# Performance work log

Hardware: AMD Instinct MI355X
Metric: run time of the kernel (lower is better)

The kernel has to match this reference:

```python
import jax, jax.numpy as jnp
import numpy as np

MAX_THRESHOLD = 0.25  # init kwarg
B, S, D, E = 8, 4096, 512, 8


def setup_inputs() -> dict:
    key = jax.random.key(0)
    ks = jax.random.split(key, 5)
    scale = 1.0 / np.sqrt(D)
    return {
        "inputs": jax.random.normal(ks[0], (B, S, D), dtype=jnp.float32),
        "W_gate": jax.random.normal(ks[1], (D, E), dtype=jnp.float32) * scale,
        "b_gate": jnp.zeros((E,), dtype=jnp.float32),
        "W_thr": jax.random.normal(ks[2], (D, 1), dtype=jnp.float32) * scale,
        "b_thr": jnp.zeros((1,), dtype=jnp.float32),
        "W_exp": jax.random.normal(ks[3], (E, D, D), dtype=jnp.float32) * scale,
        "b_exp": jnp.zeros((E, D), dtype=jnp.float32),
    }


def reference(inputs, W_gate, b_gate, W_thr, b_thr, W_exp, b_exp):
    d = inputs.shape[-1]
    x = inputs.reshape(-1, d)  # [T, D]
    # gating
    gate_logits = jax.nn.softmax(x @ W_gate + b_gate, axis=-1)          # [T, E]
    thresholds = jax.nn.sigmoid(x @ W_thr + b_thr) * MAX_THRESHOLD      # [T, 1]
    adapted = gate_logits - thresholds                                  # [T, E]
    selected = (adapted >= 0).astype(x.dtype)                           # [T, E]
    weights = adapted * selected                                        # [T, E]
    wsum = jnp.sum(weights, axis=-1, keepdims=True)
    wsum = jnp.where(wsum == 0, jnp.ones_like(wsum), wsum)
    weights = weights / wsum
    # dense-equivalent of gather->expert->scatter (weights are 0 where unselected)
    ex_out = jnp.einsum('td,edf->etf', x, W_exp) + b_exp[:, None, :]    # [E, T, D]
    results = jnp.einsum('etf,te->tf', ex_out, weights)                 # [T, D]
    return results.reshape(inputs.shape[:-1] + (results.shape[-1],))
```

## Files before the change

### kernel.cpp

```cpp
#include <hip/hip_runtime.h>


#define T_TOKENS 32768
#define DDIM 512
#define KDIM 4096
#define SLOT32 8192

typedef __attribute__((ext_vector_type(8))) short short8;
typedef __attribute__((ext_vector_type(4))) float floatx4;
typedef __bf16 bf16x2 __attribute__((ext_vector_type(2)));

__device__ __forceinline__ unsigned short f2bf(float f) {
    unsigned int u = __float_as_uint(f);
    u += 0x7FFFu + ((u >> 16) & 1u);
    return (unsigned short)(u >> 16);
}

__device__ __forceinline__ unsigned int pk2(float a, float b) {
#if __has_builtin(__builtin_amdgcn_cvt_pk_bf16_f32)
    bf16x2 v = __builtin_amdgcn_cvt_pk_bf16_f32(a, b);
    return __builtin_bit_cast(unsigned int, v);
#else
    return (unsigned int)f2bf(a) | ((unsigned int)f2bf(b) << 16);
#endif
}

__device__ __forceinline__ void async_copy16(const void* g, void* l) {
    __builtin_amdgcn_global_load_lds(
        (const __attribute__((address_space(1))) void*)g,
        (__attribute__((address_space(3))) void*)l, 16, 0, 0);
}

__device__ __forceinline__ unsigned int scale_pair(unsigned int u, float w) {
    float lo = __uint_as_float(u << 16) * w;
    float hi = __uint_as_float(u & 0xFFFF0000u) * w;
    return pk2(lo, hi);
}

__global__ __launch_bounds__(256) void gating_cvt_bt(
    const float* __restrict__ x, const float* __restrict__ Wg,
    const float* __restrict__ bg, const float* __restrict__ Wt,
    const float* __restrict__ bt, float* __restrict__ wbuf,
    unsigned short* __restrict__ Xbf,
    const float* __restrict__ Wexp, unsigned short* __restrict__ Bt)
{
    const int tid = threadIdx.x;

    if (blockIdx.x >= 512) {
        __shared__ float tile[64][65];
        const int bb = blockIdx.x - 512;
        const int k0 = (bb & 63) * 64;
        const int n0 = (bb >> 6) * 64;
        const int r = tid >> 4, cq = tid & 15;
#pragma unroll
        for (int p = 0; p < 4; ++p) {
            const int rr = p * 16 + r;
            const float4 v = *(const float4*)(Wexp + (size_t)(k0 + rr) * 512 + n0 + cq * 4);
            tile[rr][cq * 4 + 0] = v.x;
            tile[rr][cq * 4 + 1] = v.y;
            tile[rr][cq * 4 + 2] = v.z;
            tile[rr][cq * 4 + 3] = v.w;
        }
        __syncthreads();
        const int rn = tid >> 2;
        const int kq = tid & 3;
        alignas(16) unsigned short buf[16];
#pragma unroll
        for (int j = 0; j < 16; ++j) buf[j] = f2bf(tile[kq * 16 + j][rn]);
        unsigned short* dst = Bt + (size_t)(n0 + rn) * KDIM + k0 + kq * 16;
        *(uint4*)(dst) = *(const uint4*)(buf);
        *(uint4*)(dst + 8) = *(const uint4*)(buf + 8);
        return;
    }

    const int wv = tid >> 6;
    const int lane = tid & 63;

    float4 wg[16];
    {
        const float4* wgp = (const float4*)(Wg + lane * 64);
#pragma unroll
        for (int c = 0; c < 16; ++c) wg[c] = wgp[c];
    }
    const float4 wt0 = *(const float4*)(Wt + lane * 8);
    const float4 wt1 = *(const float4*)(Wt + lane * 8 + 4);
    const float bgv[8] = {bg[0], bg[1], bg[2], bg[3], bg[4], bg[5], bg[6], bg[7]};
    const float btv = bt[0];

    for (int it = 0; it < 16; ++it) {
        const int t = blockIdx.x * 64 + wv * 16 + it;
        const float* xp = x + (size_t)t * 512 + lane * 8;
        const float4 a0 = *(const float4*)(xp);
        const float4 a1 = *(const float4*)(xp + 4);

        uint2 pk0, pk1;
        pk0.x = pk2(a0.x, a0.y);
        pk0.y = pk2(a0.z, a0.w);
        pk1.x = pk2(a1.x, a1.y);
        pk1.y = pk2(a1.z, a1.w);
        uint2* xd = (uint2*)(Xbf + (size_t)t * 512 + lane * 8);
        xd[0] = pk0;
        xd[1] = pk1;

        const float xv[8] = {a0.x, a0.y, a0.z, a0.w, a1.x, a1.y, a1.z, a1.w};
        const float wtv[8] = {wt0.x, wt0.y, wt0.z, wt0.w, wt1.x, wt1.y, wt1.z, wt1.w};
        float g[9];
#pragma unroll
        for (int e = 0; e < 9; ++e) g[e] = 0.f;
#pragma unroll
        for (int j = 0; j < 8; ++j) {
            const float4 wlo = wg[j * 2];
            const float4 whi = wg[j * 2 + 1];
            g[0] = fmaf(xv[j], wlo.x, g[0]);
            g[1] = fmaf(xv[j], wlo.y, g[1]);
            g[2] = fmaf(xv[j], wlo.z, g[2]);
            g[3] = fmaf(xv[j], wlo.w, g[3]);
            g[4] = fmaf(xv[j], whi.x, g[4]);
            g[5] = fmaf(xv[j], whi.y, g[5]);
            g[6] = fmaf(xv[j], whi.z, g[6]);
            g[7] = fmaf(xv[j], whi.w, g[7]);
            g[8] = fmaf(xv[j], wtv[j], g[8]);
        }
#pragma unroll
        for (int e = 0; e < 9; ++e) {
            g[e] += __shfl_xor(g[e], 1);
            g[e] += __shfl_xor(g[e], 2);
            g[e] += __shfl_xor(g[e], 4);
            g[e] += __shfl_xor(g[e], 8);
            g[e] += __shfl_xor(g[e], 16);
            g[e] += __shfl_xor(g[e], 32);
        }
        if (lane == 0) {
#pragma unroll
            for (int e = 0; e < 8; ++e) g[e] += bgv[e];
            g[8] += btv;
            float m = g[0];
#pragma unroll
            for (int e = 1; e < 8; ++e) m = fmaxf(m, g[e]);
            float s = 0.f;
            float p[8];
#pragma unroll
            for (int e = 0; e < 8; ++e) { p[e] = __expf(g[e] - m); s += p[e]; }
            const float inv = 1.f / s;
            const float thr = 0.25f / (1.f + __expf(-g[8]));
            float w8[8];
            float ws = 0.f;
#pragma unroll
            for (int e = 0; e < 8; ++e) {
                float a = p[e] * inv - thr;
                w8[e] = a > 0.f ? a : 0.f;
                ws += w8[e];
            }
            if (ws == 0.f) ws = 1.f;
            const float invw = 1.f / ws;
            float4 o0, o1;
            o0.x = w8[0] * invw; o0.y = w8[1] * invw; o0.z = w8[2] * invw; o0.w = w8[3] * invw;
            o1.x = w8[4] * invw; o1.y = w8[5] * invw; o1.z = w8[6] * invw; o1.w = w8[7] * invw;
            float4* op = (float4*)(wbuf + (size_t)t * 8);
            op[0] = o0;
            op[1] = o1;
        }
    }
}

__global__ __launch_bounds__(512, 2) void moe_gemm(
    const unsigned short* __restrict__ Xbf, const float* __restrict__ wbuf,
    const float* __restrict__ bexp, const unsigned short* __restrict__ Bt,
    float* __restrict__ out)
{
    __shared__ alignas(16) unsigned short Bs[3 * SLOT32];
    __shared__ alignas(16) unsigned short Asl[2 * SLOT32];
    __shared__ float sWbT[8 * 256];

    const int tid = threadIdx.x;
    const int wave = tid >> 6;
    const int lane = tid & 63;
    const int wm = wave >> 2;
    const int wn = wave & 3;
    const int lm = lane & 15;
    const int lq = lane >> 4;
    const int srow = wave * 16 + (lane >> 2);
    const int pc = lane & 3;
    const int cgk = pc ^ ((lane >> 3) & 3);
    const int prd = lq ^ ((lm >> 1) & 3);

    const int lin = blockIdx.x;
    const int g = lin & 7;
    const int j_ = lin >> 3;
    const int t0 = (g * 16 + (j_ >> 1)) * 256;
    const int n0 = (j_ & 1) * 256;

    {
        const int row = tid & 255, pr = tid >> 8;
        const float4 w4 = *(const float4*)(wbuf + (size_t)(t0 + row) * 8 + pr * 4);
        sWbT[(pr * 4 + 0) * 256 + row] = w4.x;
        sWbT[(pr * 4 + 1) * 256 + row] = w4.y;
        sWbT[(pr * 4 + 2) * 256 + row] = w4.z;
        sWbT[(pr * 4 + 3) * 256 + row] = w4.w;
    }

#define STAGE_B(s_, slot_)                                                      \
    {                                                                           \
        _Pragma("unroll")                                                       \
        for (int i = 0; i < 2; ++i)                                             \
            async_copy16(Bt + (size_t)(n0 + i * 128 + srow) * KDIM + (s_) * 32 + cgk * 8, \
                         Bs + (slot_) * SLOT32 + (i * 128 + wave * 16) * 32);   \
    }
#define LOADA(s_)                                                               \
    {                                                                           \
        const int d0_ = ((s_) & 15) << 5;                                       \
        _Pragma("unroll")                                                       \
        for (int i = 0; i < 2; ++i)                                             \
            ar[i] = *(const uint4*)(Xbf + (size_t)(t0 + i * 128 + srow) * 512 + d0_ + pc * 8); \
    }
#define AWRITE(s_)                                                              \
    {                                                                           \
        const int e1 = (s_) >> 4;                                               \
        _Pragma("unroll")                                                       \
        for (int i = 0; i < 2; ++i) {                                           \
            const float w = sWbT[e1 * 256 + i * 128 + srow];                    \
            uint4 o;                                                            \
            o.x = scale_pair(ar[i].x, w);                                       \
            o.y = scale_pair(ar[i].y, w);                                       \
            o.z = scale_pair(ar[i].z, w);                                       \
            o.w = scale_pair(ar[i].w, w);                                       \
            *(uint4*)(Asl + ((s_) & 1) * SLOT32 + (i * 128 + srow) * 32 + cgk * 8) = o; \
        }                                                                       \
    }
#define READ_AF(ih)                                                             \
    {                                                                           \
        _Pragma("unroll")                                                       \
        for (int ii = 0; ii < 4; ++ii) {                                        \
            const int row = wm * 128 + ((ih) * 4 + ii) * 16 + lm;               \
            af[ii] = *(const short8*)(Ab + row * 32 + prd * 8);                 \
        }                                                                       \
    }
#define READ_B()                                                                \
    {                                                                           \
        _Pragma("unroll")                                                       \
        for (int j = 0; j < 4; ++j) {                                           \
            const int row = wn * 64 + j * 16 + lm;                              \
            b[j] = *(const short8*)(Bb + row * 32 + prd * 8);                   \
        }                                                                       \
    }
#define MFMA_H(ih)                                                              \
    {                                                                           \
        __builtin_amdgcn_s_setprio(1);                                          \
        _Pragma("unroll")                                                       \
        for (int ii = 0; ii < 4; ++ii)                                          \
            _Pragma("unroll")                                                   \
            for (int j = 0; j < 4; ++j)                                         \
                acc[(ih) * 4 + ii][j] = __builtin_amdgcn_mfma_f32_16x16x32_bf16( \
                    af[ii], b[j], acc[(ih) * 4 + ii][j], 0, 0, 0);              \
        __builtin_amdgcn_s_setprio(0);                                          \
    }

    floatx4 acc[8][4];
#pragma unroll
    for (int i = 0; i < 8; ++i)
#pragma unroll
        for (int j = 0; j < 4; ++j) acc[i][j] = (floatx4){0.f, 0.f, 0.f, 0.f};

    uint4 ar[2];

    LOADA(0);
    STAGE_B(0, 0);
    STAGE_B(1, 1);
    __syncthreads();
    AWRITE(0);
    asm volatile("s_waitcnt lgkmcnt(0)" ::: "memory");
    __builtin_amdgcn_s_barrier();

    int sl = 0;
    for (int s = 0; s < 128; ++s) {
        const unsigned short* Ab = Asl + (s & 1) * SLOT32;
        const unsigned short* Bb = Bs + sl * SLOT32;
        const int sl2 = (sl == 0) ? 2 : sl - 1;
        short8 af[4], b[4];

        READ_AF(0);
        READ_B();
        if (s < 127) LOADA(s + 1);
        if (s < 126) STAGE_B(s + 2, sl2);
        __builtin_amdgcn_s_barrier();
        MFMA_H(0);
        __builtin_amdgcn_s_barrier();

        READ_AF(1);
        if (s < 126) {
            asm volatile("s_waitcnt vmcnt(2)" ::: "memory");
        } else if (s == 126) {
            asm volatile("s_waitcnt vmcnt(0)" ::: "memory");
        }
        if (s < 127) AWRITE(s + 1);
        __builtin_amdgcn_s_barrier();
        MFMA_H(1);
        if (s < 127) asm volatile("s_waitcnt lgkmcnt(0)" ::: "memory");
        __builtin_amdgcn_s_barrier();

        sl = (sl == 2) ? 0 : sl + 1;
    }

    float bc[4][8];
#pragma unroll
    for (int j = 0; j < 4; ++j) {
        const int col = n0 + wn * 64 + j * 16 + lm;
#pragma unroll
        for (int e = 0; e < 8; ++e) bc[j][e] = bexp[e * 512 + col];
    }
#pragma unroll
    for (int i = 0; i < 8; ++i)
#pragma unroll
        for (int r = 0; r < 4; ++r) {
            const int rowl = wm * 128 + i * 16 + lq * 4 + r;
            const float4 w0 = *(const float4*)(wbuf + (size_t)(t0 + rowl) * 8);
            const float4 w1 = *(const float4*)(wbuf + (size_t)(t0 + rowl) * 8 + 4);
            float* op = out + (size_t)(t0 + rowl) * 512 + n0 + wn * 64 + lm;
#pragma unroll
            for (int j = 0; j < 4; ++j) {
                float bias = w0.x * bc[j][0];
                bias = fmaf(w0.y, bc[j][1], bias);
                bias = fmaf(w0.z, bc[j][2], bias);
                bias = fmaf(w0.w, bc[j][3], bias);
                bias = fmaf(w1.x, bc[j][4], bias);
                bias = fmaf(w1.y, bc[j][5], bias);
                bias = fmaf(w1.z, bc[j][6], bias);
                bias = fmaf(w1.w, bc[j][7], bias);
                op[j * 16] = acc[i][j][r] + bias;
            }
        }
#undef STAGE_B
#undef LOADA
#undef AWRITE
#undef READ_AF
#undef READ_B
#undef MFMA_H
}

extern "C" void kernel_launch(void* const* d_in, const int* in_sizes, int n_in,
                              void* d_out, int out_size, void* d_ws, size_t ws_size,
                              hipStream_t stream) {
    const float* x   = (const float*)d_in[0];
    const float* Wg  = (const float*)d_in[1];
    const float* bg  = (const float*)d_in[2];
    const float* Wt  = (const float*)d_in[3];
    const float* bt  = (const float*)d_in[4];
    const float* Wex = (const float*)d_in[5];
    const float* bex = (const float*)d_in[6];
    float* out = (float*)d_out;

    unsigned short* Xbf = (unsigned short*)d_ws;
    unsigned short* Bt  = (unsigned short*)((char*)d_ws + (size_t)T_TOKENS * DDIM * 2);
    float* wbuf = (float*)((char*)d_ws + (size_t)T_TOKENS * DDIM * 2
                                       + (size_t)DDIM * KDIM * 2);

    gating_cvt_bt<<<1024, 256, 0, stream>>>(x, Wg, bg, Wt, bt, wbuf, Xbf, Wex, Bt);
    moe_gemm<<<256, 512, 0, stream>>>(Xbf, wbuf, bex, Bt, out);
}
```

Baseline: 310.2 us.

## Shrink GEMM tile to 128x128 with 4-wave blocks and simple double buffering

The MoE GEMM moves from 256x256 tiles with 8 waves and a triple-buffered B pipeline to 128x128 tiles with 4 waves. Global loads are double-buffered and each k-step ends with a __syncthreads. The grid grows from 256 to 1024 blocks, so more blocks are resident and occupancy improves. The cost is lower data reuse per tile and more global traffic for A and B, plus the loss of the finer split-barrier scheduling that overlapped MFMA with loads.

```diff
diff --git a/kernel.cpp b/kernel.cpp
--- a/kernel.cpp
+++ b/kernel.cpp
@@ -4,7 +4,7 @@
 #define T_TOKENS 32768
 #define DDIM 512
 #define KDIM 4096
-#define SLOT32 8192
+#define SLOTK 4096
 
 typedef __attribute__((ext_vector_type(8))) short short8;
 typedef __attribute__((ext_vector_type(4))) float floatx4;
@@ -163,101 +163,75 @@
     }
 }
 
-__global__ __launch_bounds__(512, 2) void moe_gemm(
+__global__ __launch_bounds__(256, 4) void moe_gemm(
     const unsigned short* __restrict__ Xbf, const float* __restrict__ wbuf,
     const float* __restrict__ bexp, const unsigned short* __restrict__ Bt,
     float* __restrict__ out)
 {
-    __shared__ alignas(16) unsigned short Bs[3 * SLOT32];
-    __shared__ alignas(16) unsigned short Asl[2 * SLOT32];
-    __shared__ float sWbT[8 * 256];
+    __shared__ alignas(16) unsigned short Asl[2 * SLOTK];
+    __shared__ alignas(16) unsigned short Bsl[2 * SLOTK];
+    __shared__ float sWbT[8 * 128];
 
     const int tid = threadIdx.x;
     const int wave = tid >> 6;
     const int lane = tid & 63;
-    const int wm = wave >> 2;
-    const int wn = wave & 3;
+    const int wm = wave >> 1;
+    const int wn = wave & 1;
     const int lm = lane & 15;
     const int lq = lane >> 4;
-    const int srow = wave * 16 + (lane >> 2);
-    const int pc = lane & 3;
-    const int cgk = pc ^ ((lane >> 3) & 3);
+    const int arow = tid >> 2;
+    const int apc = tid & 3;
+    const int acg = apc ^ ((tid >> 3) & 3);
+    const int bcg = (lane & 3) ^ ((lane >> 3) & 3);
     const int prd = lq ^ ((lm >> 1) & 3);
 
     const int lin = blockIdx.x;
     const int g = lin & 7;
     const int j_ = lin >> 3;
-    const int t0 = (g * 16 + (j_ >> 1)) * 256;
-    const int n0 = (j_ & 1) * 256;
+    const int t0 = (g * 32 + (j_ >> 2)) * 128;
+    const int n0 = (j_ & 3) * 128;
 
     {
-        const int row = tid & 255, pr = tid >> 8;
-        const float4 w4 = *(const float4*)(wbuf + (size_t)(t0 + row) * 8 + pr * 4);
-        sWbT[(pr * 4 + 0) * 256 + row] = w4.x;
-        sWbT[(pr * 4 + 1) * 256 + row] = w4.y;
-        sWbT[(pr * 4 + 2) * 256 + row] = w4.z;
-        sWbT[(pr * 4 + 3) * 256 + row] = w4.w;
-    }
-
-#define STAGE_B(s_, slot_)                                                      \
-    {                                                                           \
-        _Pragma("unroll")                                                       \
-        for (int i = 0; i < 2; ++i)                                             \
-            async_copy16(Bt + (size_t)(n0 + i * 128 + srow) * KDIM + (s_) * 32 + cgk * 8, \
-                         Bs + (slot_) * SLOT32 + (i * 128 + wave * 16) * 32);   \
-    }
+        const int row = tid >> 1, half = tid & 1;
+        const float4 w4 = *(const float4*)(wbuf + (size_t)(t0 + row) * 8 + half * 4);
+        sWbT[(half * 4 + 0) * 128 + row] = w4.x;
+        sWbT[(half * 4 + 1) * 128 + row] = w4.y;
+        sWbT[(half * 4 + 2) * 128 + row] = w4.z;
+        sWbT[(half * 4 + 3) * 128 + row] = w4.w;
+    }
+
 #define LOADA(s_)                                                               \
     {                                                                           \
         const int d0_ = ((s_) & 15) << 5;                                       \
-        _Pragma("unroll")                                                       \
-        for (int i = 0; i < 2; ++i)                                             \
-            ar[i] = *(const uint4*)(Xbf + (size_t)(t0 + i * 128 + srow) * 512 + d0_ + pc * 8); \
-    }
-#define AWRITE(s_)                                                              \
+        ar[0] = *(const uint4*)(Xbf + (size_t)(t0 + arow) * 512 + d0_ + apc * 8); \
+        ar[1] = *(const uint4*)(Xbf + (size_t)(t0 + 64 + arow) * 512 + d0_ + apc * 8); \
+    }
+#define AWRITE(s_, buf_)                                                        \
     {                                                                           \
         const int e1 = (s_) >> 4;                                               \
         _Pragma("unroll")                                                       \
         for (int i = 0; i < 2; ++i) {                                           \
-            const float w = sWbT[e1 * 256 + i * 128 + srow];                    \
+            const float w = sWbT[e1 * 128 + i * 64 + arow];                     \
             uint4 o;                                                            \
             o.x = scale_pair(ar[i].x, w);                                       \
             o.y = scale_pair(ar[i].y, w);                                       \
             o.z = scale_pair(ar[i].z, w);                                       \
             o.w = scale_pair(ar[i].w, w);                                       \
-            *(uint4*)(Asl + ((s_) & 1) * SLOT32 + (i * 128 + srow) * 32 + cgk * 8) = o; \
+            *(uint4*)(Asl + (buf_) * SLOTK + (i * 64 + arow) * 32 + acg * 8) = o; \
         }                                                                       \
     }
-#define READ_AF(ih)                                                             \
+#define STAGE_B(s_, buf_)                                                       \
     {                                                                           \
         _Pragma("unroll")                                                       \
-        for (int ii = 0; ii < 4; ++ii) {                                        \
-            const int row = wm * 128 + ((ih) * 4 + ii) * 16 + lm;               \
-            af[ii] = *(const short8*)(Ab + row * 32 + prd * 8);                 \
-        }                                                                       \
-    }
-#define READ_B()                                                                \
-    {                                                                           \
-        _Pragma("unroll")                                                       \
-        for (int j = 0; j < 4; ++j) {                                           \
-            const int row = wn * 64 + j * 16 + lm;                              \
-            b[j] = *(const short8*)(Bb + row * 32 + prd * 8);                   \
-        }                                                                       \
-    }
-#define MFMA_H(ih)                                                              \
-    {                                                                           \
-        __builtin_amdgcn_s_setprio(1);                                          \
-        _Pragma("unroll")                                                       \
-        for (int ii = 0; ii < 4; ++ii)                                          \
-            _Pragma("unroll")                                                   \
-            for (int j = 0; j < 4; ++j)                                         \
-                acc[(ih) * 4 + ii][j] = __builtin_amdgcn_mfma_f32_16x16x32_bf16( \
-                    af[ii], b[j], acc[(ih) * 4 + ii][j], 0, 0, 0);              \
-        __builtin_amdgcn_s_setprio(0);                                          \
-    }
-
-    floatx4 acc[8][4];
-#pragma unroll
-    for (int i = 0; i < 8; ++i)
+        for (int i = 0; i < 2; ++i)                                             \
+            async_copy16(Bt + (size_t)(n0 + i * 64 + wave * 16 + (lane >> 2)) * KDIM \
+                             + (s_) * 32 + bcg * 8,                             \
+                         Bsl + (buf_) * SLOTK + (i * 64 + wave * 16) * 32);     \
+    }
+
+    floatx4 acc[4][4];
+#pragma unroll
+    for (int i = 0; i < 4; ++i)
 #pragma unroll
         for (int j = 0; j < 4; ++j) acc[i][j] = (floatx4){0.f, 0.f, 0.f, 0.f};
 
@@ -265,40 +239,41 @@
 
     LOADA(0);
     STAGE_B(0, 0);
-    STAGE_B(1, 1);
     __syncthreads();
-    AWRITE(0);
-    asm volatile("s_waitcnt lgkmcnt(0)" ::: "memory");
-    __builtin_amdgcn_s_barrier();
-
-    int sl = 0;
+    AWRITE(0, 0);
+    __syncthreads();
+
     for (int s = 0; s < 128; ++s) {
-        const unsigned short* Ab = Asl + (s & 1) * SLOT32;
-        const unsigned short* Bb = Bs + sl * SLOT32;
-        const int sl2 = (sl == 0) ? 2 : sl - 1;
-        short8 af[4], b[4];
-
-        READ_AF(0);
-        READ_B();
-        if (s < 127) LOADA(s + 1);
-        if (s < 126) STAGE_B(s + 2, sl2);
-        __builtin_amdgcn_s_barrier();
-        MFMA_H(0);
-        __builtin_amdgcn_s_barrier();
-
-        READ_AF(1);
-        if (s < 126) {
-            asm volatile("s_waitcnt vmcnt(2)" ::: "memory");
-        } else if (s == 126) {
-            asm volatile("s_waitcnt vmcnt(0)" ::: "memory");
-        }
-        if (s < 127) AWRITE(s + 1);
-        __builtin_amdgcn_s_barrier();
-        MFMA_H(1);
-        if (s < 127) asm volatile("s_waitcnt lgkmcnt(0)" ::: "memory");
-        __builtin_amdgcn_s_barrier();
-
-        sl = (sl == 2) ? 0 : sl + 1;
+        const int buf = s & 1;
+        if (s < 127) {
+            LOADA(s + 1);
+            STAGE_B(s + 1, buf ^ 1);
+        }
+        {
+            const unsigned short* Ab = Asl + buf * SLOTK;
+            const unsigned short* Bb = Bsl + buf * SLOTK;
+            short8 af[4], b[4];
+#pragma unroll
+            for (int ii = 0; ii < 4; ++ii) {
+                const int row = wm * 64 + ii * 16 + lm;
+                af[ii] = *(const short8*)(Ab + row * 32 + prd * 8);
+            }
+#pragma unroll
+            for (int j = 0; j < 4; ++j) {
+                const int row = wn * 64 + j * 16 + lm;
+                b[j] = *(const short8*)(Bb + row * 32 + prd * 8);
+            }
+            __builtin_amdgcn_s_setprio(1);
+#pragma unroll
+            for (int ii = 0; ii < 4; ++ii)
+#pragma unroll
+                for (int j = 0; j < 4; ++j)
+                    acc[ii][j] = __builtin_amdgcn_mfma_f32_16x16x32_bf16(
+                        af[ii], b[j], acc[ii][j], 0, 0, 0);
+            __builtin_amdgcn_s_setprio(0);
+        }
+        if (s < 127) AWRITE(s + 1, buf ^ 1);
+        __syncthreads();
     }
 
     float bc[4][8];
@@ -309,10 +284,10 @@
         for (int e = 0; e < 8; ++e) bc[j][e] = bexp[e * 512 + col];
     }
 #pragma unroll
-    for (int i = 0; i < 8; ++i)
+    for (int i = 0; i < 4; ++i)
 #pragma unroll
         for (int r = 0; r < 4; ++r) {
-            const int rowl = wm * 128 + i * 16 + lq * 4 + r;
+            const int rowl = wm * 64 + i * 16 + lq * 4 + r;
             const float4 w0 = *(const float4*)(wbuf + (size_t)(t0 + rowl) * 8);
             const float4 w1 = *(const float4*)(wbuf + (size_t)(t0 + rowl) * 8 + 4);
             float* op = out + (size_t)(t0 + rowl) * 512 + n0 + wn * 64 + lm;
@@ -329,12 +304,9 @@
                 op[j * 16] = acc[i][j][r] + bias;
             }
         }
-#undef STAGE_B
 #undef LOADA
 #undef AWRITE
-#undef READ_AF
-#undef READ_B
-#undef MFMA_H
+#undef STAGE_B
 }
 
 extern "C" void kernel_launch(void* const* d_in, const int* in_sizes, int n_in,
@@ -355,5 +327,5 @@
                                        + (size_t)DDIM * KDIM * 2);
 
     gating_cvt_bt<<<1024, 256, 0, stream>>>(x, Wg, bg, Wt, bt, wbuf, Xbf, Wex, Bt);
-    moe_gemm<<<256, 512, 0, stream>>>(Xbf, wbuf, bex, Bt, out);
-}
+    moe_gemm<<<1024, 256, 0, stream>>>(Xbf, wbuf, bex, Bt, out);
+}
```

New measurement: 322.1 us. 1.04x slower.
